# Optimization experiments

Hardware: AMD Instinct MI355X
Metric: run time of the kernel (lower is better)

Reference implementation:

```python
import jax, jax.numpy as jnp
import numpy as np

CIN = 28
HID1, HID2 = 64, 64
U_IDX, V_IDX = 11, 12
MU_U, SD_U = 0.02, 0.15
MU_V, SD_V = -0.01, 0.12


def setup_inputs() -> dict:
    key = jax.random.key(0)
    ks = jax.random.split(key, 18)
    B, T, H, W = 8, 8, 128, 128
    s = 0.05
    f32 = jnp.float32
    d = {
        "x": jax.random.normal(ks[0], (B, T, CIN, H, W), f32),
        # reduce: Conv2d(Cin, 24, 1)
        "W_red": jax.random.normal(ks[1], (24, CIN), f32) * s,
        "b_red": jnp.zeros((24,), f32),
        # l1: LSTMCell(24, HID1) + Conv2d(HID1, HID1, 1)
        "Wih1": jax.random.normal(ks[2], (4 * HID1, 24), f32) * s,
        "Whh1": jax.random.normal(ks[3], (4 * HID1, HID1), f32) * s,
        "bih1": jnp.zeros((4 * HID1,), f32),
        "bhh1": jnp.zeros((4 * HID1,), f32),
        "Wc1": jax.random.normal(ks[4], (HID1, HID1), f32) * s,
        "bc1": jnp.zeros((HID1,), f32),
        # l2: LSTMCell(HID1, HID2) + Conv2d(HID2, HID2, 1)
        "Wih2": jax.random.normal(ks[5], (4 * HID2, HID1), f32) * s,
        "Whh2": jax.random.normal(ks[6], (4 * HID2, HID2), f32) * s,
        "bih2": jnp.zeros((4 * HID2,), f32),
        "bhh2": jnp.zeros((4 * HID2,), f32),
        "Wc2": jax.random.normal(ks[7], (HID2, HID2), f32) * s,
        "bc2": jnp.zeros((HID2,), f32),
        # head: Conv2d(HID2, 1, 1)
        "W_head": jax.random.normal(ks[8], (1, HID2), f32) * s,
        "b_head": jnp.zeros((1,), f32),
    }
    return d


def _lstm_cell(flat, h, c, Wih, Whh, bih, bhh):
    # PyTorch LSTMCell gate order: i, f, g, o
    g = flat @ Wih.T + bih + h @ Whh.T + bhh
    i, f, gg, o = jnp.split(g, 4, axis=1)
    c = jax.nn.sigmoid(f) * c + jax.nn.sigmoid(i) * jnp.tanh(gg)
    h = jax.nn.sigmoid(o) * jnp.tanh(c)
    return h, c


def _conv1x1(x, W, b):
    # x: [B,C,H,W], W: [O,C]
    return jnp.einsum('bchw,oc->bohw', x, W) + b[None, :, None, None]


def reference(x, W_red, b_red, Wih1, Whh1, bih1, bhh1, Wc1, bc1,
              Wih2, Whh2, bih2, bhh2, Wc2, bc2, W_head, b_head):
    B, T, C, H, W = x.shape
    N = B * H * W
    # de-normalize u/v channels for every timestep (dropout p=0 -> identity)
    x = x.at[:, :, U_IDX].set(x[:, :, U_IDX] * SD_U + MU_U)
    x = x.at[:, :, V_IDX].set(x[:, :, V_IDX] * SD_V + MU_V)

    def step(carry, frame):
        h1, c1, h2, c2 = carry
        inp = _conv1x1(frame, W_red, b_red)                 # [B,24,H,W]
        flat1 = inp.transpose(0, 2, 3, 1).reshape(N, 24)    # pixel-wise rows
        h1, c1 = _lstm_cell(flat1, h1, c1, Wih1, Whh1, bih1, bhh1)
        h1_map = h1.reshape(B, H, W, HID1).transpose(0, 3, 1, 2)
        o1 = _conv1x1(h1_map, Wc1, bc1)                     # [B,HID1,H,W]
        flat2 = o1.transpose(0, 2, 3, 1).reshape(N, HID1)
        h2, c2 = _lstm_cell(flat2, h2, c2, Wih2, Whh2, bih2, bhh2)
        return (h1, c1, h2, c2), None

    z1 = jnp.zeros((N, HID1), x.dtype)
    z2 = jnp.zeros((N, HID2), x.dtype)
    xs = jnp.transpose(x, (1, 0, 2, 3, 4))                  # [T,B,C,H,W]
    (h1, c1, h2, c2), _ = jax.lax.scan(step, (z1, z1, z2, z2), xs)
    # only the last o2 is used by the head
    h2_map = h2.reshape(B, H, W, HID2).transpose(0, 3, 1, 2)
    o2 = _conv1x1(h2_map, Wc2, bc2)                         # [B,HID2,H,W]
    out = _conv1x1(o2, W_head, b_head)                      # [B,1,H,W]
    return out[:, 0]                                        # squeeze(1) -> [B,H,W]
```

## Files before the change

### kernel.cpp

```cpp
#include <hip/hip_runtime.h>

typedef _Float16 f16;
typedef _Float16 f16x8 __attribute__((ext_vector_type(8)));
typedef float f32x4 __attribute__((ext_vector_type(4)));

#define CIN 28
#define TT 8
#define HW 16384

#define S_SIG  (-1.44269504088896341f)
#define S_TANH ( 2.88539008177792681f)

#define WS_WX    0
#define WS_WHH1  16384
#define WS_W21   49152
#define WS_WHH2  81920
#define WS_BX    114688
#define WS_B2    115712
#define WS_WH    116736
#define WS_BH    116992

__device__ __forceinline__ float lstm_act(float gi, float gf, float gg, float go,
                                          float& c) {
  const float Ei = __builtin_amdgcn_exp2f(gi);
  const float Ef = __builtin_amdgcn_exp2f(gf);
  const float Eg = __builtin_amdgcn_exp2f(gg);
  const float Eo = __builtin_amdgcn_exp2f(go);
  const float rig = __builtin_amdgcn_rcpf((1.f + Ei) * (1.f + Eg));
  const float rf  = __builtin_amdgcn_rcpf(1.f + Ef);
  const float cn  = __builtin_fmaf(rf, c, (Eg - 1.f) * rig);
  c = cn;
  const float Ec  = __builtin_amdgcn_exp2f(cn * S_TANH);
  const float roc = __builtin_amdgcn_rcpf((1.f + Eo) * (1.f + Ec));
  return (Ec - 1.f) * roc;
}

__device__ __forceinline__ void mfma_agf(f32x4& c, f16x8 a, f16x8 b) {
  asm("s_nop 1\n\tv_mfma_f32_16x16x32_f16 %0, %1, %2, %0"
      : "+v"(c) : "v"(a), "a"(b));
}
__device__ __forceinline__ void mfma_ag(f32x4& c, f16x8 a, f16x8 b) {
  asm("v_mfma_f32_16x16x32_f16 %0, %1, %2, %0"
      : "+v"(c) : "v"(a), "a"(b));
}
__device__ __forceinline__ float ag_get(float a) {
  float v; asm("v_accvgpr_read_b32 %0, %1" : "=v"(v) : "a"(a)); return v;
}
__device__ __forceinline__ float ag_put(float v) {
  float a; asm("v_accvgpr_write_b32 %0, %1" : "=a"(a) : "v"(v)); return a;
}

__global__ __launch_bounds__(64) void prep_kernel(
    const float* __restrict__ W_red, const float* __restrict__ b_red,
    const float* __restrict__ Wih1, const float* __restrict__ Whh1,
    const float* __restrict__ bih1, const float* __restrict__ bhh1,
    const float* __restrict__ Wc1,  const float* __restrict__ bc1,
    const float* __restrict__ Wih2, const float* __restrict__ Whh2,
    const float* __restrict__ bih2, const float* __restrict__ bhh2,
    const float* __restrict__ Wc2,  const float* __restrict__ bc2,
    const float* __restrict__ W_head, const float* __restrict__ b_head,
    unsigned char* __restrict__ ws)
{
  const int g = blockIdx.x;
  const int k = threadIdx.x;
  f16* WxH   = (f16*)(ws + WS_WX);
  f16* Whh1H = (f16*)(ws + WS_WHH1);
  f16* W21H  = (f16*)(ws + WS_W21);
  f16* Whh2H = (f16*)(ws + WS_WHH2);
  float* BX  = (float*)(ws + WS_BX);
  float* B2  = (float*)(ws + WS_B2);
  float* WHp = (float*)(ws + WS_WH);
  float* BHp = (float*)(ws + WS_BH);

  const float sc = ((g >> 6) == 2) ? S_TANH : S_SIG;

  float wxv = 0.f;
  if (k < CIN) {
    float s = 0.f;
    for (int r = 0; r < 24; ++r) s += Wih1[g*24 + r] * W_red[r*28 + k];
    wxv = s;
  }
  const float wx11 = __shfl(wxv, 11, 64);
  const float wx12 = __shfl(wxv, 12, 64);
  if (k == 11) wxv *= 0.15f;
  if (k == 12) wxv *= 0.12f;
  if (k < 32) WxH[g*32 + k] = (f16)(wxv * sc);

  Whh1H[g*64 + k] = (f16)(Whh1[g*64 + k] * sc);
  Whh2H[g*64 + k] = (f16)(Whh2[g*64 + k] * sc);

  {
    float s = 0.f;
    for (int m = 0; m < 64; ++m) s += Wih2[g*64 + m] * Wc1[m*64 + k];
    W21H[g*64 + k] = (f16)(s * sc);
  }

  if (k == 0) {
    float bx = bih1[g] + bhh1[g];
    for (int r = 0; r < 24; ++r) bx += Wih1[g*24 + r] * b_red[r];
    bx += wx11 * 0.02f + wx12 * (-0.01f);
    BX[g] = bx * sc;
    float b2v = bih2[g] + bhh2[g];
    for (int m = 0; m < 64; ++m) b2v += Wih2[g*64 + m] * bc1[m];
    B2[g] = b2v * sc;
  }
  if (g == 0) {
    float s = 0.f;
    for (int m = 0; m < 64; ++m) s += W_head[m] * Wc2[m*64 + k];
    WHp[k] = s;
    if (k == 0) {
      float s2 = b_head[0];
      for (int m = 0; m < 64; ++m) s2 += W_head[m] * bc2[m];
      BHp[0] = s2;
    }
  }
}

__global__ __launch_bounds__(256)
__attribute__((amdgpu_waves_per_eu(2, 2)))
void convlstm_main(
    const float* __restrict__ x, const unsigned char* __restrict__ ws,
    float* __restrict__ out)
{
  __shared__ __align__(16) f16 xs[2][64 * 40];
  __shared__ __align__(16) f16 h1buf[2][64 * 72];
  __shared__ __align__(16) f16 h2buf[2][64 * 72];

  const int tid  = threadIdx.x;
  const int lane = tid & 63;
  const int wv   = tid >> 6;
  const int cl   = lane & 15;
  const int qd   = lane >> 4;

  const f16* WxG   = (const f16*)(ws + WS_WX);
  const f16* Whh1G = (const f16*)(ws + WS_WHH1);
  const f16* W21G  = (const f16*)(ws + WS_W21);
  const f16* Whh2G = (const f16*)(ws + WS_WHH2);
  const float* BX  = (const float*)(ws + WS_BX);
  const float* B2  = (const float*)(ws + WS_B2);

  f16x8 wxf[4], whh2v[4];
  f16x8 whh1a[4][2], w21a[4][2], whh2a[4];
  float bxr[4], b2r[4];
#pragma unroll
  for (int P = 0; P < 4; ++P) {
    const int gr = 64*P + 16*wv + cl;
    wxf[P] = *(const f16x8*)(WxG + gr*32 + qd*8);
    whh1a[P][0] = *(const f16x8*)(Whh1G + gr*64 + qd*8);
    whh1a[P][1] = *(const f16x8*)(Whh1G + gr*64 + 32 + qd*8);
    w21a[P][0]  = *(const f16x8*)(W21G  + gr*64 + qd*8);
    w21a[P][1]  = *(const f16x8*)(W21G  + gr*64 + 32 + qd*8);
    whh2a[P]    = *(const f16x8*)(Whh2G + gr*64 + qd*8);
    whh2v[P]    = *(const f16x8*)(Whh2G + gr*64 + 32 + qd*8);
    bxr[P] = BX[gr];
    b2r[P] = B2[gr];
  }

  {
    unsigned* z1 = (unsigned*)&h1buf[0][0];
    unsigned* z2 = (unsigned*)&h2buf[0][0];
#pragma unroll
    for (int i = tid; i < 2304; i += 256) { z1[i] = 0u; z2[i] = 0u; }
  }

  const int gpix = blockIdx.x * 64;
  const float* xb = x + (size_t)(gpix >> 14) * (TT * CIN * HW) + (gpix & (HW - 1));

  const int sp = lane;
  const int cb = wv * 8;

  {
    f16x8 v;
#pragma unroll
    for (int j = 0; j < 8; ++j) {
      const int ch = cb + j;
      v[j] = (ch < CIN) ? (f16)xb[ch*HW + sp] : (f16)0.f;
    }
    *(f16x8*)(&xs[0][sp*40 + cb]) = v;
  }
  __syncthreads();

  float c1s[4][4];
  float c2s[4][4];
#pragma unroll
  for (int a = 0; a < 4; ++a)
#pragma unroll
    for (int b = 0; b < 4; ++b) { c1s[a][b] = 0.f; c2s[a][b] = ag_put(0.f); }

#pragma unroll 1
  for (int t = 0; t < TT; ++t) {
    float xr[8];
    if (t + 1 < TT) {
      const float* xt = xb + (size_t)(t + 1) * (CIN * HW);
#pragma unroll
      for (int j = 0; j < 8; ++j) {
        const int ch = cb + j;
        xr[j] = (ch < CIN) ? xt[ch*HW + sp] : 0.f;
      }
    }

    const f16* xsr = xs[t & 1];
    const f16* h1r = h1buf[t & 1];
    const f16* h2r = h2buf[t & 1];
    f16* h1w = h1buf[(t + 1) & 1];
    f16* h2w = h2buf[(t + 1) & 1];

#pragma unroll
    for (int mb = 0; mb < 4; ++mb) {
      const int p = 16*mb + cl;
      const f16x8 ax  = *(const f16x8*)(xsr + p*40 + qd*8);
      const f16x8 ah0 = *(const f16x8*)(h1r + p*72 + qd*8);
      const f16x8 ah1 = *(const f16x8*)(h1r + p*72 + 32 + qd*8);
      f32x4 acc[4];
#pragma unroll
      for (int P = 0; P < 4; ++P) {
        acc[P] = (f32x4){ bxr[P], bxr[P], bxr[P], bxr[P] };
        mfma_agf(acc[P], ah0, whh1a[P][0]);
        mfma_ag (acc[P], ah1, whh1a[P][1]);
        acc[P] = __builtin_amdgcn_mfma_f32_16x16x32_f16(ax, wxf[P], acc[P], 0, 0, 0);
      }
#pragma unroll
      for (int r = 0; r < 4; ++r) {
        const float hn = lstm_act(acc[0][r], acc[1][r], acc[2][r], acc[3][r],
                                  c1s[mb][r]);
        h1w[(16*mb + 4*qd + r)*72 + 16*wv + cl] = (f16)hn;
      }
    }
    __syncthreads();

    if (t + 1 < TT) {
      f16* xsw = xs[(t + 1) & 1];
      f16x8 v;
#pragma unroll
      for (int j = 0; j < 8; ++j) v[j] = (f16)xr[j];
      *(f16x8*)(xsw + sp*40 + cb) = v;
    }

#pragma unroll
    for (int mb = 0; mb < 4; ++mb) {
      const int p = 16*mb + cl;
      const f16x8 an0 = *(const f16x8*)(h1w + p*72 + qd*8);
      const f16x8 an1 = *(const f16x8*)(h1w + p*72 + 32 + qd*8);
      const f16x8 a20 = *(const f16x8*)(h2r + p*72 + qd*8);
      const f16x8 a21 = *(const f16x8*)(h2r + p*72 + 32 + qd*8);
      f32x4 acc[4];
#pragma unroll
      for (int P = 0; P < 4; ++P) {
        acc[P] = (f32x4){ b2r[P], b2r[P], b2r[P], b2r[P] };
        mfma_agf(acc[P], an0, w21a[P][0]);
        mfma_ag (acc[P], an1, w21a[P][1]);
        mfma_ag (acc[P], a20, whh2a[P]);
        acc[P] = __builtin_amdgcn_mfma_f32_16x16x32_f16(a21, whh2v[P], acc[P], 0, 0, 0);
      }
#pragma unroll
      for (int r = 0; r < 4; ++r) {
        float co = ag_get(c2s[mb][r]);
        const float hn = lstm_act(acc[0][r], acc[1][r], acc[2][r], acc[3][r], co);
        c2s[mb][r] = ag_put(co);
        h2w[(16*mb + 4*qd + r)*72 + 16*wv + cl] = (f16)hn;
      }
    }
    __syncthreads();
  }

  if (tid < 64) {
    const float* wh = (const float*)(ws + WS_WH);
    const f16* row = &h2buf[0][tid * 72];
    float s = *((const float*)(ws + WS_BH));
#pragma unroll
    for (int k = 0; k < 64; ++k) s += (float)row[k] * wh[k];
    out[gpix + tid] = s;
  }
}

extern "C" void kernel_launch(void* const* d_in, const int* in_sizes, int n_in,
                              void* d_out, int out_size, void* d_ws, size_t ws_size,
                              hipStream_t stream) {
  const float* x      = (const float*)d_in[0];
  const float* W_red  = (const float*)d_in[1];
  const float* b_red  = (const float*)d_in[2];
  const float* Wih1   = (const float*)d_in[3];
  const float* Whh1   = (const float*)d_in[4];
  const float* bih1   = (const float*)d_in[5];
  const float* bhh1   = (const float*)d_in[6];
  const float* Wc1    = (const float*)d_in[7];
  const float* bc1    = (const float*)d_in[8];
  const float* Wih2   = (const float*)d_in[9];
  const float* Whh2   = (const float*)d_in[10];
  const float* bih2   = (const float*)d_in[11];
  const float* bhh2   = (const float*)d_in[12];
  const float* Wc2    = (const float*)d_in[13];
  const float* bc2    = (const float*)d_in[14];
  const float* W_head = (const float*)d_in[15];
  const float* b_head = (const float*)d_in[16];

  prep_kernel<<<256, 64, 0, stream>>>(W_red, b_red, Wih1, Whh1, bih1, bhh1,
                                      Wc1, bc1, Wih2, Whh2, bih2, bhh2,
                                      Wc2, bc2, W_head, b_head,
                                      (unsigned char*)d_ws);
  convlstm_main<<<2048, 256, 0, stream>>>(x, (const unsigned char*)d_ws,
                                          (float*)d_out);
}
```

Baseline: 380.7 us.

## Swap MFMA operand order so gate outputs are pixel-contiguous; vectorize h stores

Swaps the MFMA A/B operands so weights are the A operand and activations the B operand. Each lane's accumulator then holds four consecutive gates for one pixel, which allows the new h to be written as a single 4-wide f16 store instead of four scalar LDS stores. Bias is loaded as a per-lane vector, and the inline-asm AGPR weight and cell-state placement is dropped in favour of compiler builtins. The LSTM activation is rewritten to use one fewer reciprocal per element, and next-frame inputs are converted to f16 at load time. The trade-off is higher VGPR pressure now that weights and cell state no longer sit in AGPRs.

```diff
diff --git a/kernel.cpp b/kernel.cpp
--- a/kernel.cpp
+++ b/kernel.cpp
@@ -1,6 +1,7 @@
 #include <hip/hip_runtime.h>
 
 typedef _Float16 f16;
+typedef _Float16 f16x4 __attribute__((ext_vector_type(4)));
 typedef _Float16 f16x8 __attribute__((ext_vector_type(8)));
 typedef float f32x4 __attribute__((ext_vector_type(4)));
 
@@ -26,28 +27,15 @@
   const float Ef = __builtin_amdgcn_exp2f(gf);
   const float Eg = __builtin_amdgcn_exp2f(gg);
   const float Eo = __builtin_amdgcn_exp2f(go);
-  const float rig = __builtin_amdgcn_rcpf((1.f + Ei) * (1.f + Eg));
-  const float rf  = __builtin_amdgcn_rcpf(1.f + Ef);
-  const float cn  = __builtin_fmaf(rf, c, (Eg - 1.f) * rig);
+  const float pig = (1.f + Ei) * (1.f + Eg);
+  const float pf  = 1.f + Ef;
+  const float r3  = __builtin_amdgcn_rcpf(pig * pf);
+  const float t1  = (Eg - 1.f) * pf;
+  const float cn  = r3 * __builtin_fmaf(pig, c, t1);
   c = cn;
   const float Ec  = __builtin_amdgcn_exp2f(cn * S_TANH);
   const float roc = __builtin_amdgcn_rcpf((1.f + Eo) * (1.f + Ec));
   return (Ec - 1.f) * roc;
-}
-
-__device__ __forceinline__ void mfma_agf(f32x4& c, f16x8 a, f16x8 b) {
-  asm("s_nop 1\n\tv_mfma_f32_16x16x32_f16 %0, %1, %2, %0"
-      : "+v"(c) : "v"(a), "a"(b));
-}
-__device__ __forceinline__ void mfma_ag(f32x4& c, f16x8 a, f16x8 b) {
-  asm("v_mfma_f32_16x16x32_f16 %0, %1, %2, %0"
-      : "+v"(c) : "v"(a), "a"(b));
-}
-__device__ __forceinline__ float ag_get(float a) {
-  float v; asm("v_accvgpr_read_b32 %0, %1" : "=v"(v) : "a"(a)); return v;
-}
-__device__ __forceinline__ float ag_put(float v) {
-  float a; asm("v_accvgpr_write_b32 %0, %1" : "=a"(a) : "v"(v)); return a;
 }
 
 __global__ __launch_bounds__(64) void prep_kernel(
@@ -139,21 +127,23 @@
   const float* BX  = (const float*)(ws + WS_BX);
   const float* B2  = (const float*)(ws + WS_B2);
 
-  f16x8 wxf[4], whh2v[4];
-  f16x8 whh1a[4][2], w21a[4][2], whh2a[4];
-  float bxr[4], b2r[4];
+  f16x8 wx[4];
+  f16x8 whh1k0[4], whh1k1[4];
+  f16x8 w21k0[4],  w21k1[4];
+  f16x8 whh2k0[4], whh2k1[4];
+  f32x4 bxq[4], b2q[4];
 #pragma unroll
   for (int P = 0; P < 4; ++P) {
     const int gr = 64*P + 16*wv + cl;
-    wxf[P] = *(const f16x8*)(WxG + gr*32 + qd*8);
-    whh1a[P][0] = *(const f16x8*)(Whh1G + gr*64 + qd*8);
-    whh1a[P][1] = *(const f16x8*)(Whh1G + gr*64 + 32 + qd*8);
-    w21a[P][0]  = *(const f16x8*)(W21G  + gr*64 + qd*8);
-    w21a[P][1]  = *(const f16x8*)(W21G  + gr*64 + 32 + qd*8);
-    whh2a[P]    = *(const f16x8*)(Whh2G + gr*64 + qd*8);
-    whh2v[P]    = *(const f16x8*)(Whh2G + gr*64 + 32 + qd*8);
-    bxr[P] = BX[gr];
-    b2r[P] = B2[gr];
+    wx[P]     = *(const f16x8*)(WxG + gr*32 + qd*8);
+    whh1k0[P] = *(const f16x8*)(Whh1G + gr*64 + qd*8);
+    whh1k1[P] = *(const f16x8*)(Whh1G + gr*64 + 32 + qd*8);
+    w21k0[P]  = *(const f16x8*)(W21G  + gr*64 + qd*8);
+    w21k1[P]  = *(const f16x8*)(W21G  + gr*64 + 32 + qd*8);
+    whh2k0[P] = *(const f16x8*)(Whh2G + gr*64 + qd*8);
+    whh2k1[P] = *(const f16x8*)(Whh2G + gr*64 + 32 + qd*8);
+    bxq[P] = *(const f32x4*)(BX + 64*P + 16*wv + 4*qd);
+    b2q[P] = *(const f32x4*)(B2 + 64*P + 16*wv + 4*qd);
   }
 
   {
@@ -185,17 +175,17 @@
 #pragma unroll
   for (int a = 0; a < 4; ++a)
 #pragma unroll
-    for (int b = 0; b < 4; ++b) { c1s[a][b] = 0.f; c2s[a][b] = ag_put(0.f); }
+    for (int b = 0; b < 4; ++b) { c1s[a][b] = 0.f; c2s[a][b] = 0.f; }
 
 #pragma unroll 1
   for (int t = 0; t < TT; ++t) {
-    float xr[8];
+    f16x8 xrv;
     if (t + 1 < TT) {
       const float* xt = xb + (size_t)(t + 1) * (CIN * HW);
 #pragma unroll
       for (int j = 0; j < 8; ++j) {
         const int ch = cb + j;
-        xr[j] = (ch < CIN) ? xt[ch*HW + sp] : 0.f;
+        xrv[j] = (ch < CIN) ? (f16)xt[ch*HW + sp] : (f16)0.f;
       }
     }
 
@@ -214,26 +204,23 @@
       f32x4 acc[4];
 #pragma unroll
       for (int P = 0; P < 4; ++P) {
-        acc[P] = (f32x4){ bxr[P], bxr[P], bxr[P], bxr[P] };
-        mfma_agf(acc[P], ah0, whh1a[P][0]);
-        mfma_ag (acc[P], ah1, whh1a[P][1]);
-        acc[P] = __builtin_amdgcn_mfma_f32_16x16x32_f16(ax, wxf[P], acc[P], 0, 0, 0);
+        acc[P] = __builtin_amdgcn_mfma_f32_16x16x32_f16(whh1k0[P], ah0, bxq[P], 0, 0, 0);
+        acc[P] = __builtin_amdgcn_mfma_f32_16x16x32_f16(whh1k1[P], ah1, acc[P], 0, 0, 0);
+        acc[P] = __builtin_amdgcn_mfma_f32_16x16x32_f16(wx[P],     ax,  acc[P], 0, 0, 0);
       }
-#pragma unroll
-      for (int r = 0; r < 4; ++r) {
-        const float hn = lstm_act(acc[0][r], acc[1][r], acc[2][r], acc[3][r],
-                                  c1s[mb][r]);
-        h1w[(16*mb + 4*qd + r)*72 + 16*wv + cl] = (f16)hn;
-      }
+      float hn[4];
+#pragma unroll
+      for (int r = 0; r < 4; ++r)
+        hn[r] = lstm_act(acc[0][r], acc[1][r], acc[2][r], acc[3][r], c1s[mb][r]);
+      f16x4 hv; hv[0] = (f16)hn[0]; hv[1] = (f16)hn[1];
+      hv[2] = (f16)hn[2]; hv[3] = (f16)hn[3];
+      *(f16x4*)(h1w + p*72 + 16*wv + 4*qd) = hv;
     }
     __syncthreads();
 
     if (t + 1 < TT) {
       f16* xsw = xs[(t + 1) & 1];
-      f16x8 v;
-#pragma unroll
-      for (int j = 0; j < 8; ++j) v[j] = (f16)xr[j];
-      *(f16x8*)(xsw + sp*40 + cb) = v;
+      *(f16x8*)(xsw + sp*40 + cb) = xrv;
     }
 
 #pragma unroll
@@ -246,19 +233,18 @@
       f32x4 acc[4];
 #pragma unroll
       for (int P = 0; P < 4; ++P) {
-        acc[P] = (f32x4){ b2r[P], b2r[P], b2r[P], b2r[P] };
-        mfma_agf(acc[P], an0, w21a[P][0]);
-        mfma_ag (acc[P], an1, w21a[P][1]);
-        mfma_ag (acc[P], a20, whh2a[P]);
-        acc[P] = __builtin_amdgcn_mfma_f32_16x16x32_f16(a21, whh2v[P], acc[P], 0, 0, 0);
+        acc[P] = __builtin_amdgcn_mfma_f32_16x16x32_f16(w21k0[P],  an0, b2q[P], 0, 0, 0);
+        acc[P] = __builtin_amdgcn_mfma_f32_16x16x32_f16(w21k1[P],  an1, acc[P], 0, 0, 0);
+        acc[P] = __builtin_amdgcn_mfma_f32_16x16x32_f16(whh2k0[P], a20, acc[P], 0, 0, 0);
+        acc[P] = __builtin_amdgcn_mfma_f32_16x16x32_f16(whh2k1[P], a21, acc[P], 0, 0, 0);
       }
-#pragma unroll
-      for (int r = 0; r < 4; ++r) {
-        float co = ag_get(c2s[mb][r]);
-        const float hn = lstm_act(acc[0][r], acc[1][r], acc[2][r], acc[3][r], co);
-        c2s[mb][r] = ag_put(co);
-        h2w[(16*mb + 4*qd + r)*72 + 16*wv + cl] = (f16)hn;
-      }
+      float hn[4];
+#pragma unroll
+      for (int r = 0; r < 4; ++r)
+        hn[r] = lstm_act(acc[0][r], acc[1][r], acc[2][r], acc[3][r], c2s[mb][r]);
+      f16x4 hv; hv[0] = (f16)hn[0]; hv[1] = (f16)hn[1];
+      hv[2] = (f16)hn[2]; hv[3] = (f16)hn[3];
+      *(f16x4*)(h2w + p*72 + 16*wv + 4*qd) = hv;
     }
     __syncthreads();
   }
```

New measurement: 435.9 us. +14.5%, slower.
